# Performance work log

Measured on AMD Instinct MI355X. Metric: run time of the kernel, lower is better.

## Reference

```python
import jax, jax.numpy as jnp
import numpy as np
from functools import reduce

N_QUBITS = 8
DEPTH = 2
DIM = 2 ** N_QUBITS  # state-vector dimension
HIDDEN = 512


def _cnot_chain_np(n):
    # product of CNOT(w, w+1) for w = 0..n-2, wire 0 = most-significant bit (PennyLane order)
    C4 = np.array([[1, 0, 0, 0], [0, 1, 0, 0], [0, 0, 0, 1], [0, 0, 1, 0]], dtype=np.complex64)
    U = np.eye(2 ** n, dtype=np.complex64)
    for w in range(n - 1):
        full = np.kron(np.kron(np.eye(2 ** w, dtype=np.complex64), C4),
                       np.eye(2 ** (n - w - 2), dtype=np.complex64))
        U = full @ U
    return U

CNOT_CHAIN = jnp.asarray(_cnot_chain_np(N_QUBITS))
# PauliZ on wire 0 (MSB): +1 for basis states with MSB=0, -1 otherwise
Z0 = jnp.asarray(np.where(np.arange(DIM) < DIM // 2, 1.0, -1.0).astype(np.float32))


def _rot(p):
    # PennyLane Rot(phi, theta, omega) = RZ(omega) @ RY(theta) @ RZ(phi)
    phi, th, om = p[0], p[1], p[2]
    c = jnp.cos(th / 2).astype(jnp.complex64)
    s = jnp.sin(th / 2).astype(jnp.complex64)
    ep = jnp.exp(-0.5j * (phi + om).astype(jnp.complex64))  # e^{-i(phi+om)/2}
    em = jnp.exp(0.5j * (phi - om).astype(jnp.complex64))   # e^{ i(phi-om)/2}
    m00 = ep * c
    m01 = -em * s
    m10 = jnp.conj(em) * s
    m11 = jnp.conj(ep) * c
    return jnp.stack([jnp.stack([m00, m01]), jnp.stack([m10, m11])])


def _gate_unitary(P):
    # P: (depth, n_qubits, 3). Circuit (after data RX): per layer Rot on every wire, then CNOT chain.
    U = jnp.eye(DIM, dtype=jnp.complex64)
    for l in range(DEPTH):
        layer = reduce(jnp.kron, [_rot(P[l, w]) for w in range(N_QUBITS)])
        U = CNOT_CHAIN @ (layer @ U)
    return U


def _expval(theta, U):
    # RX(theta)|0...0> = cos(t/2)|0..0> - i sin(t/2)|10..0>; then fixed unitary U; <Z_0>
    col0 = U[:, 0]          # U |00...0>
    col1 = U[:, DIM // 2]   # U |10...0>
    a = jnp.cos(theta / 2)[:, None]
    b = jnp.sin(theta / 2)[:, None]
    psi = a * col0[None, :] - 1j * b * col1[None, :]  # (B, DIM)
    return jnp.sum(Z0 * (psi.real ** 2 + psi.imag ** 2), axis=-1)  # (B,)


def setup_inputs() -> dict:
    key = jax.random.key(0)
    ks = jax.random.split(key, 13)
    T, B, D, H, Q = 256, 128, 512, HIDDEN, N_QUBITS
    inp = {"inputs": jax.random.normal(ks[0], (T, B, D), jnp.float32)}
    for i, g in enumerate(["f", "i", "g", "o"]):
        inp[f"W{g}"] = jax.random.normal(ks[1 + 3 * i], (Q, D + H), jnp.float32) * 0.02
        inp[f"b{g}"] = jnp.zeros((Q,), jnp.float32)
        inp[f"P{g}"] = jax.random.normal(ks[3 + 3 * i], (DEPTH, Q, 3), jnp.float32)
    return inp


def reference(inputs, Wf, bf, Pf, Wi, bi, Pi, Wg, bg, Pg, Wo, bo, Po):
    Uf, Ui, Ug, Uo = _gate_unitary(Pf), _gate_unitary(Pi), _gate_unitary(Pg), _gate_unitary(Po)

    def step(carry, x):
        hx, cx = carry
        comb = jnp.concatenate([x, hx], axis=1)  # (B, D+H)
        f = jax.nn.sigmoid(_expval((comb @ Wf.T + bf)[:, 0], Uf))[:, None]
        i = jax.nn.sigmoid(_expval((comb @ Wi.T + bi)[:, 0], Ui))[:, None]
        g = jnp.tanh(_expval((comb @ Wg.T + bg)[:, 0], Ug))[:, None]
        o = jax.nn.sigmoid(_expval((comb @ Wo.T + bo)[:, 0], Uo))[:, None]
        cx = f * cx + i * g
        hx = o * jnp.tanh(cx)
        return (hx, cx), hx

    B = inputs.shape[1]
    init = (jnp.zeros((B, HIDDEN), inputs.dtype), jnp.zeros((B, HIDDEN), inputs.dtype))
    (hx, cx), outputs = jax.lax.scan(step, init, inputs)
    return outputs, hx, cx
```

## Files before the change

kernel.cpp:

```cpp
#include <hip/hip_runtime.h>
#include <math.h>

#define T_STEPS 256
#define BATCH   128
#define DIMD    512
#define NROWS   (T_STEPS * BATCH)
#define PF      16
#define WRITER_BLOCKS 258
#define GEMV_BLOCKS 2048

#define INV2PI  0.15915494309189535f
#define L2E     1.4426950408889634f
#define TWO_L2E 2.8853900817779268f

#define AGENT __HIP_MEMORY_SCOPE_AGENT

typedef float f32x4 __attribute__((ext_vector_type(4)));

#if __has_builtin(__builtin_amdgcn_sinf)
#define HW_SIN(x) __builtin_amdgcn_sinf(x)
#else
__device__ __forceinline__ float HW_SIN(float x) { return __sinf(x * 6.283185307179586f); }
#endif
#if __has_builtin(__builtin_amdgcn_exp2f)
#define EXP2(x) __builtin_amdgcn_exp2f(x)
#else
#define EXP2(x) exp2f(x)
#endif
#if __has_builtin(__builtin_amdgcn_rcpf)
#define RCP(x) __builtin_amdgcn_rcpf(x)
#else
#define RCP(x) (1.0f / (x))
#endif

__device__ __forceinline__ void  st_rlx(float* p, float v) {
    __hip_atomic_store(p, v, __ATOMIC_RELAXED, AGENT);
}
__device__ __forceinline__ void  st_rlx_i(int* p, int v) {
    __hip_atomic_store(p, v, __ATOMIC_RELAXED, AGENT);
}
__device__ __forceinline__ int   ld_rlx_i(const int* p) {
    return __hip_atomic_load(p, __ATOMIC_RELAXED, AGENT);
}
#define VMFENCE() asm volatile("s_waitcnt vmcnt(0)" ::: "memory")
#define CFENCE()  asm volatile("" ::: "memory")

__global__ __launch_bounds__(256) void prep(
    const float* __restrict__ inp,
    const float* __restrict__ Wf, const float* __restrict__ Wi,
    const float* __restrict__ Wg, const float* __restrict__ Wo,
    const float* __restrict__ bfp, const float* __restrict__ bip,
    const float* __restrict__ bgp, const float* __restrict__ bop,
    const float* __restrict__ Pf, const float* __restrict__ Pi,
    const float* __restrict__ Pg, const float* __restrict__ Po,
    float* __restrict__ gc, int* __restrict__ hProg,
    float4* __restrict__ X4)
{
    const int bid  = blockIdx.x;
    const int wv   = threadIdx.x >> 6;
    const int lane = threadIdx.x & 63;

    if (bid == 0) {
        if (threadIdx.x == 0) { hProg[0] = 0; hProg[1] = 0; }
        const int g = wv;
        const float* P = (g == 0) ? Pf : (g == 1) ? Pi : (g == 2) ? Pg : Po;
        const float* W = (g == 0) ? Wf : (g == 1) ? Wi : (g == 2) ? Wg : Wo;

        __shared__ float s0r[4][256], s0i[4][256], s1r[4][256], s1i[4][256];

#pragma unroll
        for (int j = 0; j < 4; ++j) {
            const int k = lane + 64 * j;
            s0r[g][k] = (k == 0)   ? 1.0f : 0.0f;  s0i[g][k] = 0.0f;
            s1r[g][k] = (k == 128) ? 1.0f : 0.0f;  s1i[g][k] = 0.0f;
        }
        __syncthreads();

        for (int l = 0; l < 2; ++l) {
            for (int w = 0; w < 8; ++w) {
                const float phi = P[l * 24 + w * 3 + 0];
                const float th  = P[l * 24 + w * 3 + 1];
                const float om  = P[l * 24 + w * 3 + 2];
                float sh, chh; __sincosf(0.5f * th, &sh, &chh);
                float sp, cp;  __sincosf(0.5f * (phi + om), &sp, &cp);
                float sm, cm;  __sincosf(0.5f * (phi - om), &sm, &cm);
                const float m00r =  cp * chh, m00i = -sp * chh;
                const float m01r = -cm * sh,  m01i = -sm * sh;
                const float m10r =  cm * sh,  m10i = -sm * sh;
                const float m11r =  cp * chh, m11i =  sp * chh;

                const int shift = 7 - w;
                const int mask  = 1 << shift;

                float n0r[4], n0i[4], n1r[4], n1i[4];
#pragma unroll
                for (int j = 0; j < 4; ++j) {
                    const int k  = lane + 64 * j;
                    const int bit = (k >> shift) & 1;
                    const int i0 = k & ~mask, i1 = k | mask;
                    const float a0r = s0r[g][i0], a0i = s0i[g][i0];
                    const float a1r = s0r[g][i1], a1i = s0i[g][i1];
                    const float b0r = s1r[g][i0], b0i = s1i[g][i0];
                    const float b1r = s1r[g][i1], b1i = s1i[g][i1];
                    const float mr0 = bit ? m10r : m00r, mi0 = bit ? m10i : m00i;
                    const float mr1 = bit ? m11r : m01r, mi1 = bit ? m11i : m01i;
                    n0r[j] = mr0 * a0r - mi0 * a0i + mr1 * a1r - mi1 * a1i;
                    n0i[j] = mr0 * a0i + mi0 * a0r + mr1 * a1i + mi1 * a1r;
                    n1r[j] = mr0 * b0r - mi0 * b0i + mr1 * b1r - mi1 * b1i;
                    n1i[j] = mr0 * b0i + mi0 * b0r + mr1 * b1i + mi1 * b1r;
                }
                __syncthreads();
#pragma unroll
                for (int j = 0; j < 4; ++j) {
                    const int k = lane + 64 * j;
                    s0r[g][k] = n0r[j]; s0i[g][k] = n0i[j];
                    s1r[g][k] = n1r[j]; s1i[g][k] = n1i[j];
                }
                __syncthreads();
            }
            float n0r[4], n0i[4], n1r[4], n1i[4];
#pragma unroll
            for (int j = 0; j < 4; ++j) {
                int src = lane + 64 * j;
                for (int w = 6; w >= 0; --w) {
                    const int cb = (src >> (7 - w)) & 1;
                    src ^= cb << (6 - w);
                }
                n0r[j] = s0r[g][src]; n0i[j] = s0i[g][src];
                n1r[j] = s1r[g][src]; n1i[j] = s1i[g][src];
            }
            __syncthreads();
#pragma unroll
            for (int j = 0; j < 4; ++j) {
                const int k = lane + 64 * j;
                s0r[g][k] = n0r[j]; s0i[g][k] = n0i[j];
                s1r[g][k] = n1r[j]; s1i[g][k] = n1i[j];
            }
            __syncthreads();
        }

        float t00 = 0, t11 = 0, t01 = 0;
#pragma unroll
        for (int j = 0; j < 4; ++j) {
            const int k = lane + 64 * j;
            const float z = (k < 128) ? 1.0f : -1.0f;
            t00 += z * (s0r[g][k] * s0r[g][k] + s0i[g][k] * s0i[g][k]);
            t11 += z * (s1r[g][k] * s1r[g][k] + s1i[g][k] * s1i[g][k]);
            t01 += z * (s0i[g][k] * s1r[g][k] - s0r[g][k] * s1i[g][k]);
        }
        float tsw = 0;
#pragma unroll
        for (int j = 0; j < 8; ++j) tsw += W[512 + lane + 64 * j];

        for (int off = 32; off; off >>= 1) {
            t00 += __shfl_xor(t00, off);
            t11 += __shfl_xor(t11, off);
            t01 += __shfl_xor(t01, off);
            tsw += __shfl_xor(tsw, off);
        }
        if (lane == 0) {
            const float A  = 0.5f * (t00 + t11);
            const float Bc = 0.5f * (t00 - t11);
            const float Bs = -t01;
            const float R  = sqrtf(Bc * Bc + Bs * Bs);
            const float ph = atan2f(Bc, Bs) * INV2PI;
            const float sc = (g == 2) ? TWO_L2E : -L2E;
            gc[4 * g + 0] = sc * A;
            gc[4 * g + 1] = sc * R;
            gc[4 * g + 2] = ph;
            gc[4 * g + 3] = tsw * INV2PI;
        }
        return;
    }

    const int rowbase = (bid - 1) * 16 + wv * 4;

    const float4* wfp = (const float4*)Wf;
    const float4* wip = (const float4*)Wi;
    const float4* wgp = (const float4*)Wg;
    const float4* wop = (const float4*)Wo;
    const float4 fa = wfp[lane], fb = wfp[lane + 64];
    const float4 ia = wip[lane], ib = wip[lane + 64];
    const float4 ga = wgp[lane], gb = wgp[lane + 64];
    const float4 oa = wop[lane], ob = wop[lane + 64];

    const float4* xr = (const float4*)(inp + (size_t)rowbase * DIMD);
    float sums[4][4];
#pragma unroll
    for (int r = 0; r < 4; ++r) {
        const float4 xa = xr[r * 128 + lane];
        const float4 xb = xr[r * 128 + lane + 64];
        sums[r][0] = xa.x * fa.x + xa.y * fa.y + xa.z * fa.z + xa.w * fa.w
                   + xb.x * fb.x + xb.y * fb.y + xb.z * fb.z + xb.w * fb.w;
        sums[r][1] = xa.x * ia.x + xa.y * ia.y + xa.z * ia.z + xa.w * ia.w
                   + xb.x * ib.x + xb.y * ib.y + xb.z * ib.z + xb.w * ib.w;
        sums[r][2] = xa.x * ga.x + xa.y * ga.y + xa.z * ga.z + xa.w * ga.w
                   + xb.x * gb.x + xb.y * gb.y + xb.z * gb.z + xb.w * gb.w;
        sums[r][3] = xa.x * oa.x + xa.y * oa.y + xa.z * oa.z + xa.w * oa.w
                   + xb.x * ob.x + xb.y * ob.y + xb.z * ob.z + xb.w * ob.w;
    }
#pragma unroll
    for (int r = 0; r < 4; ++r)
#pragma unroll
        for (int g = 0; g < 4; ++g)
            for (int off = 32; off; off >>= 1)
                sums[r][g] += __shfl_xor(sums[r][g], off);

    if (lane == 0) {
        const float b0f = bfp[0], b0i = bip[0], b0g = bgp[0], b0o = bop[0];
#pragma unroll
        for (int r = 0; r < 4; ++r) {
            X4[rowbase + r] = make_float4((sums[r][0] + b0f) * INV2PI,
                                          (sums[r][1] + b0i) * INV2PI,
                                          (sums[r][2] + b0g) * INV2PI,
                                          (sums[r][3] + b0o) * INV2PI);
        }
    }
}

__global__ __launch_bounds__(256) void scan_write(
    const float4* __restrict__ X4, const float* __restrict__ gc,
    float* __restrict__ Hs, float* __restrict__ cfin,
    float4* __restrict__ out4, int* __restrict__ hProg)
{
    const int bid  = blockIdx.x;
    const int wv   = threadIdx.x >> 6;
    const int lane = threadIdx.x & 63;

    if (bid == 0) {
        if (threadIdx.x >= BATCH) return;
        const int b = threadIdx.x;

        const float Af = gc[0],  Rf = gc[1],  phf = gc[2],  swf = gc[3];
        const float Ai = gc[4],  Ri = gc[5],  phi_ = gc[6], swi = gc[7];
        const float Ag = gc[8],  Rg = gc[9],  phg = gc[10], swg = gc[11];
        const float Ao = gc[12], Ro = gc[13], pho = gc[14], swo = gc[15];

        float4 p[PF];
#pragma unroll
        for (int j = 0; j < PF; ++j) {
            const float4 v = X4[j * BATCH + b];
            p[j] = make_float4(v.x + phf, v.y + phi_, v.z + phg, v.w + pho);
        }

        float c = 0.0f, h = 0.0f;
        for (int tb = 0; tb < T_STEPS; tb += PF) {
#pragma unroll
            for (int j = 0; j < PF; ++j) {
                const int t = tb + j;
                const float4 xv = p[j];
                {
                    const float4 v = X4[(t + PF) * BATCH + b];
                    p[j] = make_float4(v.x + phf, v.y + phi_,
                                       v.z + phg, v.w + pho);
                }
                const float thf = fmaf(h, swf, xv.x);
                const float thi = fmaf(h, swi, xv.y);
                const float thg = fmaf(h, swg, xv.z);
                const float tho = fmaf(h, swo, xv.w);
                const float ef = EXP2(fmaf(Rf, HW_SIN(thf), Af));
                const float ei = EXP2(fmaf(Ri, HW_SIN(thi), Ai));
                const float eg = EXP2(fmaf(Rg, HW_SIN(thg), Ag));
                const float eo = EXP2(fmaf(Ro, HW_SIN(tho), Ao));
                const float Ff = ef + 1.0f, Fi = ei + 1.0f;
                const float Fg = eg + 1.0f, Fo = eo + 1.0f;
                const float FiFg = Fi * Fg;
                const float num  = fmaf(c, FiFg, (eg - 1.0f) * Ff);
                c = num * RCP(Ff * FiFg);
                const float ec = EXP2(c * TWO_L2E);
                h = (ec - 1.0f) * RCP(Fo * (ec + 1.0f));
                st_rlx(&Hs[t * BATCH + b], h);
            }
            if (tb == T_STEPS - PF) st_rlx(&cfin[b], c);
            if (((tb + PF) & 31) == 0) {
                VMFENCE();
                if (lane == 0) st_rlx_i(&hProg[wv], tb + PF);
            }
        }
        return;
    }

    const int t  = bid - 1;
    const int qd = wv;
    const int pidx = (qd < 2) ? 0 : 1;
    const int need = (t < 256) ? (t + 1) : 256;

    int cur = ld_rlx_i(&hProg[pidx]);
    while (cur < need) {
        int chunks = ((need - cur) >> 4) + 1;
        for (int s = 0; s < chunks; ++s) __builtin_amdgcn_s_sleep(16);
        cur = ld_rlx_i(&hProg[pidx]);
    }
    CFENCE();

    const float* src = (t == 257) ? cfin : (Hs + ((t >= 256 ? 255 : t) * BATCH));
    const float hv = src[qd * 32 + (lane & 31)];

    size_t base = (t < 256) ? ((size_t)t * 16384)
                : (t == 256 ? (size_t)4194304 : (size_t)4210688);
    base += (size_t)qd * 4096;
#pragma unroll 8
    for (int j = 0; j < 64; ++j) {
        const float v = __shfl(hv, j >> 1);
        const f32x4 val = {v, v, v, v};
        __builtin_nontemporal_store(val, (f32x4*)(out4 + base + j * 64 + lane));
    }
}

extern "C" void kernel_launch(void* const* d_in, const int* in_sizes, int n_in,
                              void* d_out, int out_size, void* d_ws, size_t ws_size,
                              hipStream_t stream)
{
    const float* inp = (const float*)d_in[0];
    const float* Wf  = (const float*)d_in[1];
    const float* bfv = (const float*)d_in[2];
    const float* Pf  = (const float*)d_in[3];
    const float* Wi  = (const float*)d_in[4];
    const float* biv = (const float*)d_in[5];
    const float* Pi  = (const float*)d_in[6];
    const float* Wg  = (const float*)d_in[7];
    const float* bgv = (const float*)d_in[8];
    const float* Pg  = (const float*)d_in[9];
    const float* Wo  = (const float*)d_in[10];
    const float* bov = (const float*)d_in[11];
    const float* Po  = (const float*)d_in[12];

    float4* X4   = (float4*)d_ws;
    float*  Hs   = (float*)(X4 + NROWS + PF * BATCH);
    float*  cfin = Hs + NROWS;
    float*  gc   = cfin + BATCH;
    int*    hProg = (int*)(gc + 16);

    prep<<<1 + GEMV_BLOCKS, 256, 0, stream>>>(inp, Wf, Wi, Wg, Wo,
                                              bfv, biv, bgv, bov,
                                              Pf, Pi, Pg, Po,
                                              gc, hProg, X4);
    scan_write<<<1 + WRITER_BLOCKS, 256, 0, stream>>>(X4, gc, Hs, cfin,
                                                      (float4*)d_out, hProg);
}
```

Baseline: 54.09 us.

## Split gate evaluation across 4 lanes per batch with DPP quad broadcast

The serial scan block now runs 512 threads, with four lanes per batch element. Each lane evaluates one gate's sin/exp2, and the four values are shared through DPP quad broadcasts, which shortens the per-step transcendental critical path. Writer blocks are merged so each 512-thread block handles two timesteps. The progress flag is reduced to a single counter published after __syncthreads, and the sleep backoff is longer. The cost is a block-wide barrier every 32 steps and four times the active lanes for the recurrence.

```diff
diff --git a/kernel.cpp b/kernel.cpp
--- a/kernel.cpp
+++ b/kernel.cpp
@@ -6,8 +6,8 @@
 #define DIMD    512
 #define NROWS   (T_STEPS * BATCH)
 #define PF      16
-#define WRITER_BLOCKS 258
 #define GEMV_BLOCKS 2048
+#define WRITER_BLOCKS 129
 
 #define INV2PI  0.15915494309189535f
 #define L2E     1.4426950408889634f
@@ -33,6 +33,21 @@
 #define RCP(x) (1.0f / (x))
 #endif
 
+#if __has_builtin(__builtin_amdgcn_mov_dpp)
+template <int CTRL>
+__device__ __forceinline__ float quad_bcast(float x) {
+    int xi = __builtin_bit_cast(int, x);
+    int r  = __builtin_amdgcn_mov_dpp(xi, CTRL, 0xF, 0xF, true);
+    return __builtin_bit_cast(float, r);
+}
+#else
+template <int CTRL>
+__device__ __forceinline__ float quad_bcast(float x) {
+    const int src = (threadIdx.x & ~3) + (CTRL & 3);
+    return __shfl(x, src & 63);
+}
+#endif
+
 __device__ __forceinline__ void  st_rlx(float* p, float v) {
     __hip_atomic_store(p, v, __ATOMIC_RELAXED, AGENT);
 }
@@ -42,7 +57,6 @@
 __device__ __forceinline__ int   ld_rlx_i(const int* p) {
     return __hip_atomic_load(p, __ATOMIC_RELAXED, AGENT);
 }
-#define VMFENCE() asm volatile("s_waitcnt vmcnt(0)" ::: "memory")
 #define CFENCE()  asm volatile("" ::: "memory")
 
 __global__ __launch_bounds__(256) void prep(
@@ -218,78 +232,72 @@
     }
 }
 
-__global__ __launch_bounds__(256) void scan_write(
-    const float4* __restrict__ X4, const float* __restrict__ gc,
+__global__ __launch_bounds__(512) void scan_write(
+    const float* __restrict__ Xs, const float* __restrict__ gc,
     float* __restrict__ Hs, float* __restrict__ cfin,
     float4* __restrict__ out4, int* __restrict__ hProg)
 {
     const int bid  = blockIdx.x;
-    const int wv   = threadIdx.x >> 6;
-    const int lane = threadIdx.x & 63;
+    const int tid  = threadIdx.x;
+    const int wv   = tid >> 6;
+    const int lane = tid & 63;
 
     if (bid == 0) {
-        if (threadIdx.x >= BATCH) return;
-        const int b = threadIdx.x;
-
-        const float Af = gc[0],  Rf = gc[1],  phf = gc[2],  swf = gc[3];
-        const float Ai = gc[4],  Ri = gc[5],  phi_ = gc[6], swi = gc[7];
-        const float Ag = gc[8],  Rg = gc[9],  phg = gc[10], swg = gc[11];
-        const float Ao = gc[12], Ro = gc[13], pho = gc[14], swo = gc[15];
-
-        float4 p[PF];
-#pragma unroll
-        for (int j = 0; j < PF; ++j) {
-            const float4 v = X4[j * BATCH + b];
-            p[j] = make_float4(v.x + phf, v.y + phi_, v.z + phg, v.w + pho);
-        }
+        const int g  = tid & 3;
+        const int cb = tid >> 2;
+        const float A  = gc[4 * g + 0];
+        const float R  = gc[4 * g + 1];
+        const float ph = gc[4 * g + 2];
+        const float sw = gc[4 * g + 3];
+
+        float p[PF];
+#pragma unroll
+        for (int j = 0; j < PF; ++j) p[j] = Xs[j * 512 + tid] + ph;
 
         float c = 0.0f, h = 0.0f;
         for (int tb = 0; tb < T_STEPS; tb += PF) {
 #pragma unroll
             for (int j = 0; j < PF; ++j) {
                 const int t = tb + j;
-                const float4 xv = p[j];
-                {
-                    const float4 v = X4[(t + PF) * BATCH + b];
-                    p[j] = make_float4(v.x + phf, v.y + phi_,
-                                       v.z + phg, v.w + pho);
-                }
-                const float thf = fmaf(h, swf, xv.x);
-                const float thi = fmaf(h, swi, xv.y);
-                const float thg = fmaf(h, swg, xv.z);
-                const float tho = fmaf(h, swo, xv.w);
-                const float ef = EXP2(fmaf(Rf, HW_SIN(thf), Af));
-                const float ei = EXP2(fmaf(Ri, HW_SIN(thi), Ai));
-                const float eg = EXP2(fmaf(Rg, HW_SIN(thg), Ag));
-                const float eo = EXP2(fmaf(Ro, HW_SIN(tho), Ao));
-                const float Ff = ef + 1.0f, Fi = ei + 1.0f;
-                const float Fg = eg + 1.0f, Fo = eo + 1.0f;
+                const float xv = p[j];
+                p[j] = Xs[(t + PF) * 512 + tid] + ph;
+
+                const float th = fmaf(h, sw, xv);
+                const float e  = EXP2(fmaf(R, HW_SIN(th), A));
+                const float vf = quad_bcast<0x00>(e);
+                const float vi = quad_bcast<0x55>(e);
+                const float vg = quad_bcast<0xAA>(e);
+                const float vo = quad_bcast<0xFF>(e);
+                const float Ff = vf + 1.0f, Fi = vi + 1.0f;
+                const float Fg = vg + 1.0f, Fo = vo + 1.0f;
                 const float FiFg = Fi * Fg;
-                const float num  = fmaf(c, FiFg, (eg - 1.0f) * Ff);
+                const float num  = fmaf(c, FiFg, (vg - 1.0f) * Ff);
                 c = num * RCP(Ff * FiFg);
                 const float ec = EXP2(c * TWO_L2E);
                 h = (ec - 1.0f) * RCP(Fo * (ec + 1.0f));
-                st_rlx(&Hs[t * BATCH + b], h);
-            }
-            if (tb == T_STEPS - PF) st_rlx(&cfin[b], c);
+                if (g == 0) st_rlx(&Hs[t * BATCH + cb], h);
+            }
+            if (tb == T_STEPS - PF && g == 0) st_rlx(&cfin[cb], c);
             if (((tb + PF) & 31) == 0) {
-                VMFENCE();
-                if (lane == 0) st_rlx_i(&hProg[wv], tb + PF);
+                __syncthreads();
+                if (tid == 0) st_rlx_i(&hProg[0], tb + PF);
             }
         }
         return;
     }
 
-    const int t  = bid - 1;
-    const int qd = wv;
-    const int pidx = (qd < 2) ? 0 : 1;
+    const int t  = 2 * (bid - 1) + (wv >> 2);
+    const int qd = wv & 3;
     const int need = (t < 256) ? (t + 1) : 256;
 
-    int cur = ld_rlx_i(&hProg[pidx]);
+    int cur = ld_rlx_i(&hProg[0]);
     while (cur < need) {
-        int chunks = ((need - cur) >> 4) + 1;
-        for (int s = 0; s < chunks; ++s) __builtin_amdgcn_s_sleep(16);
-        cur = ld_rlx_i(&hProg[pidx]);
+        int loops = ((need - cur) >> 5) + 1;
+        for (int s = 0; s < loops; ++s) {
+            __builtin_amdgcn_s_sleep(32);
+            __builtin_amdgcn_s_sleep(32);
+        }
+        cur = ld_rlx_i(&hProg[0]);
     }
     CFENCE();
 
@@ -335,6 +343,7 @@
                                               bfv, biv, bgv, bov,
                                               Pf, Pi, Pg, Po,
                                               gc, hProg, X4);
-    scan_write<<<1 + WRITER_BLOCKS, 256, 0, stream>>>(X4, gc, Hs, cfin,
+    scan_write<<<1 + WRITER_BLOCKS, 512, 0, stream>>>((const float*)X4, gc,
+                                                      Hs, cfin,
                                                       (float4*)d_out, hProg);
 }
```

After: 62.46 us. +15.5%, slower.

## Batch-prefetch input chunk per block and coarsen writer progress signalling

Applied to the files above, without the earlier changes.

The serial scan thread now issues all PF loads for the next chunk at the start of each block into a separate register array, then converts them at the end, instead of interleaving one load per step. Progress flags are published every 64 steps instead of every 32, and writer blocks wait for the matching 64-step boundary with longer sleep intervals. This is meant to take load latency and fences off the recurrence critical path and to cut polling traffic. The cost is more registers for the second buffer and later start times for writer blocks.

```diff
diff --git a/kernel.cpp b/kernel.cpp
--- a/kernel.cpp
+++ b/kernel.cpp
@@ -236,7 +236,7 @@
         const float Ag = gc[8],  Rg = gc[9],  phg = gc[10], swg = gc[11];
         const float Ao = gc[12], Ro = gc[13], pho = gc[14], swo = gc[15];
 
-        float4 p[PF];
+        float4 p[PF], q[PF];
 #pragma unroll
         for (int j = 0; j < PF; ++j) {
             const float4 v = X4[j * BATCH + b];
@@ -244,16 +244,13 @@
         }
 
         float c = 0.0f, h = 0.0f;
-        for (int tb = 0; tb < T_STEPS; tb += PF) {
+        for (int k = 0; k < T_STEPS / PF; ++k) {
+            const int tb = k * PF;
+#pragma unroll
+            for (int j = 0; j < PF; ++j) q[j] = X4[(tb + PF + j) * BATCH + b];
 #pragma unroll
             for (int j = 0; j < PF; ++j) {
-                const int t = tb + j;
                 const float4 xv = p[j];
-                {
-                    const float4 v = X4[(t + PF) * BATCH + b];
-                    p[j] = make_float4(v.x + phf, v.y + phi_,
-                                       v.z + phg, v.w + pho);
-                }
                 const float thf = fmaf(h, swf, xv.x);
                 const float thi = fmaf(h, swi, xv.y);
                 const float thg = fmaf(h, swg, xv.z);
@@ -269,12 +266,17 @@
                 c = num * RCP(Ff * FiFg);
                 const float ec = EXP2(c * TWO_L2E);
                 h = (ec - 1.0f) * RCP(Fo * (ec + 1.0f));
-                st_rlx(&Hs[t * BATCH + b], h);
-            }
-            if (tb == T_STEPS - PF) st_rlx(&cfin[b], c);
-            if (((tb + PF) & 31) == 0) {
+                st_rlx(&Hs[(tb + j) * BATCH + b], h);
+            }
+            if (k == T_STEPS / PF - 1) st_rlx(&cfin[b], c);
+            if ((k & 3) == 3) {
                 VMFENCE();
                 if (lane == 0) st_rlx_i(&hProg[wv], tb + PF);
+            }
+#pragma unroll
+            for (int j = 0; j < PF; ++j) {
+                p[j] = make_float4(q[j].x + phf, q[j].y + phi_,
+                                   q[j].z + phg, q[j].w + pho);
             }
         }
         return;
@@ -283,12 +285,15 @@
     const int t  = bid - 1;
     const int qd = wv;
     const int pidx = (qd < 2) ? 0 : 1;
-    const int need = (t < 256) ? (t + 1) : 256;
+    const int need = (t < 256) ? ((t >> 6) + 1) << 6 : 256;
 
     int cur = ld_rlx_i(&hProg[pidx]);
     while (cur < need) {
-        int chunks = ((need - cur) >> 4) + 1;
-        for (int s = 0; s < chunks; ++s) __builtin_amdgcn_s_sleep(16);
+        int loops = ((need - cur) >> 5) + 1;
+        for (int s = 0; s < loops; ++s) {
+            __builtin_amdgcn_s_sleep(32);
+            __builtin_amdgcn_s_sleep(32);
+        }
         cur = ld_rlx_i(&hProg[pidx]);
     }
     CFENCE();
```

After: 55.19 us. 2.0% more time.
